# Performance work log

Measured on AMD Instinct MI355X. Metric: run time of the kernel, lower is better.

## Reference

```python
import jax, jax.numpy as jnp
import numpy as np

EMBED_DIM = 1024
ATTN_DIM = 1024
BATCH = 4
SEQ = 2048


def setup_inputs() -> dict:
    key = jax.random.key(0)
    k1, k2, k3, k4 = jax.random.split(key, 4)
    embedded = jax.random.normal(k1, (BATCH, SEQ, EMBED_DIM), dtype=jnp.float32)
    # torch Linear weights have shape [out_features, in_features]
    scale = 1.0 / np.sqrt(EMBED_DIM)
    W_K = jax.random.uniform(k2, (ATTN_DIM, EMBED_DIM), dtype=jnp.float32, minval=-scale, maxval=scale)
    W_Q = jax.random.uniform(k3, (ATTN_DIM, EMBED_DIM), dtype=jnp.float32, minval=-scale, maxval=scale)
    W_V = jax.random.uniform(k4, (ATTN_DIM, EMBED_DIM), dtype=jnp.float32, minval=-scale, maxval=scale)
    return {"embedded": embedded, "W_K": W_K, "W_Q": W_Q, "W_V": W_V}


def reference(embedded, W_K, W_Q, W_V):
    # embedded: [B, L, E]; W_*: [A, E] (torch Linear layout, applied as x @ W.T)
    L = embedded.shape[1]
    A = W_K.shape[0]
    K = jnp.einsum('ble,ae->bla', embedded, W_K)
    Q = jnp.einsum('ble,ae->bla', embedded, W_Q)
    V = jnp.einsum('ble,ae->bla', embedded, W_V)
    att = jnp.einsum('bqa,bka->bqk', Q, K) / jnp.sqrt(jnp.float32(A))  # [B, L, L]
    causal = jnp.tril(jnp.ones((L, L), dtype=bool))  # lower-triangular mask
    att = jnp.where(causal, att, -jnp.inf)
    att = jax.nn.softmax(att, axis=-1)
    return jnp.einsum('bqk,bka->bqa', att, V)
```

## Files before the change

kernel.cpp:

```cpp
#include <hip/hip_runtime.h>
#include <hip/hip_bf16.h>
#include <stdint.h>

#define BATCH 4
#define SEQ   2048
#define EMB   1024
#define ADIM  1024

typedef __attribute__((ext_vector_type(8))) short  short8;
typedef __attribute__((ext_vector_type(4))) float  float4v;

static __device__ __forceinline__ unsigned short f2bf(float f) {
    unsigned int u = __float_as_uint(f);
    u += 0x7FFFu + ((u >> 16) & 1u);
    return (unsigned short)(u >> 16);
}

static __device__ __forceinline__ uint2 pack4(float4v v) {
    uint2 r;
    r.x = (unsigned)f2bf(v.x) | ((unsigned)f2bf(v.y) << 16);
    r.y = (unsigned)f2bf(v.z) | ((unsigned)f2bf(v.w) << 16);
    return r;
}

static __device__ __forceinline__ void gload16(const void* g, void* l) {
    __builtin_amdgcn_global_load_lds(
        (const __attribute__((address_space(1))) void*)g,
        (__attribute__((address_space(3))) void*)l, 16, 0, 0);
}

static __device__ __forceinline__ int swz8(int row) { return ((row >> 1) & 3) << 3; }

__global__ __launch_bounds__(256) void prep_kernel(
    const float* __restrict__ X,  const float* __restrict__ Wv,
    const float* __restrict__ Wq, const float* __restrict__ Wk,
    unsigned short* __restrict__ Xb, unsigned short* __restrict__ Wvb,
    unsigned short* __restrict__ WqT, unsigned short* __restrict__ WkT,
    float* __restrict__ rowsum, float* __restrict__ out)
{
    __shared__ unsigned short T[64][72];
    const int bI = blockIdx.x;
    if (bI < 4608) {
        const float* src; unsigned short* dst; int off;
        if (bI < 4096) { src = X;  dst = Xb;  off = bI; }
        else           { src = Wv; dst = Wvb; off = bI - 4096; }
        const int i = (off * 256 + threadIdx.x) * 8;
        float4v a = *(const float4v*)(src + i);
        float4v b = *(const float4v*)(src + i + 4);
        uint2 pa = pack4(a), pb = pack4(b);
        uint4 o; o.x = pa.x; o.y = pa.y; o.z = pb.x; o.w = pb.y;
        *(uint4*)(dst + i) = o;
        return;
    }
    if (bI < 4616) {
        const int i = ((bI - 4608) * 256 + threadIdx.x) * 4;
        *(float4v*)(rowsum + i) = float4v{0.f, 0.f, 0.f, 0.f};
        return;
    }
    if (bI >= 5128) {
        const int o   = bI - 5128;
        const int b   = o >> 11;
        const int row = o & 2047;
        float* dst = out + ((size_t)(b * 2048 + row) * 1024) + threadIdx.x * 4;
        *(float4v*)dst = float4v{0.f, 0.f, 0.f, 0.f};
        return;
    }
    const int z    = (bI - 4616) >> 8;
    const int tile = (bI - 4616) & 255;
    const int ti = tile >> 4;
    const int tj = tile & 15;
    const float* W = z ? Wk : Wq;
    unsigned short* WT = z ? WkT : WqT;
    const int t  = threadIdx.x;
    const int r  = t >> 2;
    const int c  = (t & 3) << 4;

    const float* src = W + (size_t)(ti * 64 + r) * EMB + tj * 64 + c;
    #pragma unroll
    for (int u = 0; u < 4; ++u) {
        float4v v = *(const float4v*)(src + 4 * u);
        uint2 p = pack4(v);
        *(uint2*)&T[r][c + 4 * u] = p;
    }
    __syncthreads();
    unsigned short tmp[16];
    #pragma unroll
    for (int u = 0; u < 16; ++u) tmp[u] = T[c + u][r];
    unsigned short* dst = WT + (size_t)(tj * 64 + r) * EMB + ti * 64 + c;
    *(uint4*)(dst)     = *(uint4*)&tmp[0];
    *(uint4*)(dst + 8) = *(uint4*)&tmp[8];
}

static __device__ __forceinline__ void gemm_core(
    const unsigned short* __restrict__ A, const unsigned short* __restrict__ B,
    int lda, int ldb, int m0, int n0, int klen,
    unsigned short* As, unsigned short* Bs, float4v acc[4][4])
{
    const int tid  = threadIdx.x;
    const int r    = tid >> 2;
    const int c8   = ((tid & 3) << 3) ^ swz8(tid >> 2);
    const int lane = tid & 63;
    const int wave = tid >> 6;
    const int quad = lane >> 4;
    const int l16  = lane & 15;
    const int wm   = (wave >> 1) << 6;
    const int wn   = (wave & 1) << 6;

    const unsigned short* Ag = A + (size_t)(m0 + r) * lda + c8;
    const unsigned short* Bg = B + (size_t)(n0 + r) * ldb + c8;
    unsigned short* Al = As + tid * 8;
    unsigned short* Bl = Bs + tid * 8;
    const int niter = klen >> 5;

    #define ISSUE_A(k0, st) do { \
        unsigned short* al_ = Al + (st) * 4096; \
        gload16(Ag + (k0),                    al_); \
        gload16(Ag + (k0) + (size_t)64 * lda, al_ + 2048); \
    } while (0)
    #define ISSUE_B(k0, st) do { \
        unsigned short* bl_ = Bl + (st) * 4096; \
        gload16(Bg + (k0),                    bl_); \
        gload16(Bg + (k0) + (size_t)64 * ldb, bl_ + 2048); \
    } while (0)

    ISSUE_A(0, 0);  ISSUE_B(0, 0);
    ISSUE_A(32, 1); ISSUE_B(32, 1);

    int ci = 0, ii = 2;
    for (int it = 0; it < niter; ++it) {
        const int knext = (it + 2 < niter) ? ((it + 2) << 5) : 0;
        const unsigned short* Ah = As + ci * 4096;
        const unsigned short* Bh = Bs + ci * 4096;
        short8 bfr[4];

        ISSUE_A(knext, ii);
        asm volatile("s_waitcnt vmcnt(6)" ::: "memory");
        asm volatile("s_barrier" ::: "memory");
        {
            short8 af0, af1;
            {
                const int row = wm + l16;
                af0 = *(const short8*)&Ah[row * 32 + ((quad * 8) ^ swz8(row))];
            }
            {
                const int row = wm + 16 + l16;
                af1 = *(const short8*)&Ah[row * 32 + ((quad * 8) ^ swz8(row))];
            }
            #pragma unroll
            for (int j = 0; j < 4; ++j) {
                const int row = wn + 16 * j + l16;
                bfr[j] = *(const short8*)&Bh[row * 32 + ((quad * 8) ^ swz8(row))];
            }
            __builtin_amdgcn_s_setprio(1);
            #pragma unroll
            for (int j = 0; j < 4; ++j)
                acc[0][j] = __builtin_amdgcn_mfma_f32_16x16x32_bf16(af0, bfr[j], acc[0][j], 0, 0, 0);
            #pragma unroll
            for (int j = 0; j < 4; ++j)
                acc[1][j] = __builtin_amdgcn_mfma_f32_16x16x32_bf16(af1, bfr[j], acc[1][j], 0, 0, 0);
            __builtin_amdgcn_s_setprio(0);
        }
        asm volatile("s_barrier" ::: "memory");

        ISSUE_B(knext, ii);
        {
            short8 af2, af3;
            {
                const int row = wm + 32 + l16;
                af2 = *(const short8*)&Ah[row * 32 + ((quad * 8) ^ swz8(row))];
            }
            {
                const int row = wm + 48 + l16;
                af3 = *(const short8*)&Ah[row * 32 + ((quad * 8) ^ swz8(row))];
            }
            __builtin_amdgcn_s_setprio(1);
            #pragma unroll
            for (int j = 0; j < 4; ++j)
                acc[2][j] = __builtin_amdgcn_mfma_f32_16x16x32_bf16(af2, bfr[j], acc[2][j], 0, 0, 0);
            #pragma unroll
            for (int j = 0; j < 4; ++j)
                acc[3][j] = __builtin_amdgcn_mfma_f32_16x16x32_bf16(af3, bfr[j], acc[3][j], 0, 0, 0);
            __builtin_amdgcn_s_setprio(0);
        }
        asm volatile("s_barrier" ::: "memory");
        ci = (ci == 2) ? 0 : ci + 1;
        ii = (ii == 2) ? 0 : ii + 1;
    }
    asm volatile("s_waitcnt vmcnt(0)" ::: "memory");
    #undef ISSUE_A
    #undef ISSUE_B
}

#define DECL_TILE_IDX() \
    const int lane = threadIdx.x & 63; \
    const int wave = threadIdx.x >> 6; \
    const int quad = lane >> 4; \
    const int l16  = lane & 15; \
    const int wm   = (wave >> 1) << 6; \
    const int wn   = (wave & 1) << 6;

__global__ __launch_bounds__(256, 3) void m_kernel(
    const unsigned short* __restrict__ WkT, const unsigned short* __restrict__ WqT,
    float* __restrict__ Mtf)
{
    __shared__ __align__(16) unsigned short As[3 * 128 * 32];
    __shared__ __align__(16) unsigned short Bs[3 * 128 * 32];
    const int idx = blockIdx.x;
    const int kc  = idx >> 6;
    const int t   = idx & 63;
    const int m0  = (t >> 3) << 7;
    const int n0  = (t & 7) << 7;

    float4v acc[4][4];
    #pragma unroll
    for (int i = 0; i < 4; ++i)
        #pragma unroll
        for (int j = 0; j < 4; ++j)
            acc[i][j] = float4v{0.f, 0.f, 0.f, 0.f};

    gemm_core(WkT + kc * 256, WqT + kc * 256, EMB, EMB, m0, n0, 256, As, Bs, acc);

    float* dst = Mtf + (size_t)kc * 1024 * 1024;
    DECL_TILE_IDX();
    #pragma unroll
    for (int i = 0; i < 4; ++i)
        #pragma unroll
        for (int j = 0; j < 4; ++j)
            #pragma unroll
            for (int rr = 0; rr < 4; ++rr) {
                const int row = m0 + wm + 16 * i + quad * 4 + rr;
                const int col = n0 + wn + 16 * j + l16;
                dst[(size_t)row * EMB + col] = acc[i][j][rr];
            }
}

__global__ __launch_bounds__(256) void mc_kernel(
    const float* __restrict__ Mtf, unsigned short* __restrict__ Mt)
{
    const int base = (blockIdx.x * 256 + threadIdx.x) * 16;
    #pragma unroll
    for (int u = 0; u < 4; ++u) {
        const int i = base + u * 4;
        float4v s = *(const float4v*)(Mtf + i);
        s = s + *(const float4v*)(Mtf + 1048576 + i);
        s = s + *(const float4v*)(Mtf + 2097152 + i);
        s = s + *(const float4v*)(Mtf + 3145728 + i);
        s = s * 0.03125f;
        uint2 p = pack4(s);
        *(uint2*)(Mt + i) = p;
    }
}

__global__ __launch_bounds__(512, 2) void qv_kernel(
    const unsigned short* __restrict__ Xb, const unsigned short* __restrict__ Mt,
    const unsigned short* __restrict__ Wvb,
    unsigned short* __restrict__ Qpb, unsigned short* __restrict__ Vtb)
{
    __shared__ __align__(16) unsigned short LDS[49152];
    unsigned short* As = LDS;
    unsigned short* Bs = LDS + 24576;

    const int idx  = blockIdx.x;
    const int mt   = ((idx & 7) << 2) | ((idx >> 3) & 3);
    const int slot = idx >> 5;
    const int z    = slot >> 2;
    const int n0   = (slot & 3) << 8;
    const int m0   = mt << 8;
    const unsigned short* B = z ? Wvb : Mt;

    const int tid  = threadIdx.x;
    const int lane = tid & 63;
    const int wave = tid >> 6;
    const int quad = lane >> 4;
    const int l16  = lane & 15;
    const int wm   = (wave >> 2) << 7;
    const int wn   = (wave & 3) << 6;

    const int srow = tid >> 2;
    const int c8   = ((tid & 3) << 3) ^ swz8(srow);

    const unsigned short* Ag0 = Xb + (size_t)(m0 + srow) * EMB + c8;
    const unsigned short* Ag1 = Ag0 + (size_t)128 * EMB;
    const unsigned short* Bg0 = B  + (size_t)(n0 + srow) * EMB + c8;
    const unsigned short* Bg1 = Bg0 + (size_t)128 * EMB;
    unsigned short* Al = As + tid * 8;
    unsigned short* Bl = Bs + tid * 8;

    #define ISSUE_QA(t, st) do { \
        gload16(Ag0 + (t) * 32, Al + (st) * 8192); \
        gload16(Ag1 + (t) * 32, Al + (st) * 8192 + 4096); \
    } while (0)
    #define ISSUE_QB(t, st) do { \
        gload16(Bg0 + (t) * 32, Bl + (st) * 8192); \
        gload16(Bg1 + (t) * 32, Bl + (st) * 8192 + 4096); \
    } while (0)

    float4v acc[8][4];
    #pragma unroll
    for (int i = 0; i < 8; ++i)
        #pragma unroll
        for (int j = 0; j < 4; ++j)
            acc[i][j] = float4v{0.f, 0.f, 0.f, 0.f};

    ISSUE_QA(0, 0); ISSUE_QB(0, 0);
    ISSUE_QA(1, 1); ISSUE_QB(1, 1);

    int ci = 0, ii = 2;
    for (int it = 0; it < 32; ++it) {
        const int tn = (it + 2 < 32) ? (it + 2) : 0;
        const unsigned short* Ah = As + ci * 8192;
        const unsigned short* Bh = Bs + ci * 8192;
        short8 bfr[4];

        ISSUE_QA(tn, ii);
        asm volatile("s_waitcnt vmcnt(6)" ::: "memory");
        asm volatile("s_barrier" ::: "memory");
        {
            short8 af[4];
            #pragma unroll
            for (int i = 0; i < 4; ++i) {
                const int row = wm + 16 * i + l16;
                af[i] = *(const short8*)&Ah[row * 32 + ((quad * 8) ^ swz8(row))];
            }
            #pragma unroll
            for (int j = 0; j < 4; ++j) {
                const int row = wn + 16 * j + l16;
                bfr[j] = *(const short8*)&Bh[row * 32 + ((quad * 8) ^ swz8(row))];
            }
            __builtin_amdgcn_s_setprio(1);
            #pragma unroll
            for (int i = 0; i < 4; ++i)
                #pragma unroll
                for (int j = 0; j < 4; ++j)
                    acc[i][j] = __builtin_amdgcn_mfma_f32_16x16x32_bf16(af[i], bfr[j], acc[i][j], 0, 0, 0);
            __builtin_amdgcn_s_setprio(0);
        }
        asm volatile("s_barrier" ::: "memory");

        ISSUE_QB(tn, ii);
        {
            short8 af[4];
            #pragma unroll
            for (int i = 0; i < 4; ++i) {
                const int row = wm + 64 + 16 * i + l16;
                af[i] = *(const short8*)&Ah[row * 32 + ((quad * 8) ^ swz8(row))];
            }
            __builtin_amdgcn_s_setprio(1);
            #pragma unroll
            for (int i = 0; i < 4; ++i)
                #pragma unroll
                for (int j = 0; j < 4; ++j)
                    acc[i + 4][j] = __builtin_amdgcn_mfma_f32_16x16x32_bf16(af[i], bfr[j], acc[i + 4][j], 0, 0, 0);
            __builtin_amdgcn_s_setprio(0);
        }
        asm volatile("s_barrier" ::: "memory");
        ci = (ci == 2) ? 0 : ci + 1;
        ii = (ii == 2) ? 0 : ii + 1;
    }
    asm volatile("s_waitcnt vmcnt(0)" ::: "memory");
    #undef ISSUE_QA
    #undef ISSUE_QB

    if (z == 0) {
        #pragma unroll
        for (int i = 0; i < 8; ++i)
            #pragma unroll
            for (int j = 0; j < 4; ++j)
                #pragma unroll
                for (int rr = 0; rr < 4; ++rr) {
                    const int row = m0 + wm + ((i & 3) << 4) + ((i >> 2) << 6) + quad * 4 + rr;
                    const int col = n0 + wn + 16 * j + l16;
                    Qpb[(size_t)row * ADIM + col] = f2bf(acc[i][j][rr]);
                }
    } else {
        const int bb = m0 >> 11;
        const int l0 = m0 & (SEQ - 1);
        #pragma unroll
        for (int h = 0; h < 2; ++h) {
            __syncthreads();
            if ((wm >> 7) == h) {
                #pragma unroll
                for (int i = 0; i < 8; ++i)
                    #pragma unroll
                    for (int j = 0; j < 4; ++j) {
                        const int qloc = ((i & 3) << 4) + ((i >> 2) << 6) + quad * 4;
                        const int acol = wn + 16 * j + l16;
                        uint2 w;
                        w.x = (unsigned)f2bf(acc[i][j][0]) | ((unsigned)f2bf(acc[i][j][1]) << 16);
                        w.y = (unsigned)f2bf(acc[i][j][2]) | ((unsigned)f2bf(acc[i][j][3]) << 16);
                        *(uint2*)&LDS[acol * 136 + qloc] = w;
                    }
            }
            __syncthreads();
            const int acol = tid >> 1;
            const int qh   = (tid & 1) << 6;
            unsigned short* dst = Vtb + (((size_t)(bb * ADIM + n0 + acol)) << 11)
                                      + l0 + h * 128 + qh;
            #pragma unroll
            for (int u = 0; u < 8; ++u)
                *(uint4*)(dst + u * 8) = *(const uint4*)&LDS[acol * 136 + qh + u * 8];
        }
    }
}

__global__ __launch_bounds__(256, 3) void s_kernel(
    const unsigned short* __restrict__ Qpb, const unsigned short* __restrict__ Xb,
    unsigned short* __restrict__ E, float* __restrict__ rowsum)
{
    const int idx = blockIdx.x;
    const int x   = idx & 7;
    const int j   = idx >> 3;
    const int b   = j / 17;
    const int u   = j - b * 17;
    const int qt  = (u <= x) ? x : 15 - x;
    const int kt  = (u <= x) ? u : u - (x + 1);
    const int q0  = qt << 7;
    const int k0  = kt << 7;

    __shared__ __align__(16) unsigned short As[3 * 128 * 32];
    __shared__ __align__(16) unsigned short Bs[3 * 128 * 32];

    float4v acc[4][4];
    #pragma unroll
    for (int i = 0; i < 4; ++i)
        #pragma unroll
        for (int jj = 0; jj < 4; ++jj)
            acc[i][jj] = float4v{0.f, 0.f, 0.f, 0.f};

    gemm_core(Qpb + (size_t)b * SEQ * ADIM, Xb + (size_t)b * SEQ * EMB,
              ADIM, EMB, q0, k0, EMB, As, Bs, acc);

    unsigned short* Eb = E + (size_t)b * SEQ * SEQ;
    float* rsb = rowsum + (size_t)b * SEQ;
    DECL_TILE_IDX();
    #pragma unroll
    for (int i = 0; i < 4; ++i)
        #pragma unroll
        for (int rr = 0; rr < 4; ++rr) {
            const int row = q0 + wm + 16 * i + quad * 4 + rr;
            float s = 0.f;
            #pragma unroll
            for (int jj = 0; jj < 4; ++jj) {
                const int col = k0 + wn + 16 * jj + l16;
                float e = (col <= row) ? __expf(acc[i][jj][rr]) : 0.f;
                s += e;
                Eb[(size_t)row * SEQ + col] = f2bf(e);
            }
            s += __shfl_xor(s, 1);
            s += __shfl_xor(s, 2);
            s += __shfl_xor(s, 4);
            s += __shfl_xor(s, 8);
            if (l16 == 0) atomicAdd(&rsb[row], s);
        }
}

__global__ __launch_bounds__(256, 3) void pv_kernel(
    const unsigned short* __restrict__ E, const unsigned short* __restrict__ Vtb,
    const float* __restrict__ rowsum, float* __restrict__ out)
{
    const int idx = blockIdx.x;
    const int x   = idx & 7;
    const int j   = idx >> 3;
    const int c   = j >> 5;
    const int col = j & 31;
    const int b   = col >> 3;
    const int a0  = (col & 7) << 7;

    const int ea  = (x + 1) << 2;
    const int g0  = (c == 0) ? 0 : ((c == 1) ? 23 : 46);
    const int g1  = (c == 2) ? 68 : (g0 + 23);

    __shared__ __align__(16) unsigned short As[3 * 128 * 32];
    __shared__ __align__(16) unsigned short Bs[3 * 128 * 32];

    const unsigned short* Eb = E   + (size_t)b * SEQ * SEQ;
    const unsigned short* Vb = Vtb + (size_t)b * ADIM * SEQ;
    float* ob = out + (size_t)b * SEQ * ADIM;
    const float* rsb = rowsum + (size_t)b * SEQ;
    DECL_TILE_IDX();

    #pragma unroll
    for (int seg = 0; seg < 2; ++seg) {
        const int lo = seg ? ea : 0;
        const int hi = seg ? 68 : ea;
        const int s0 = (g0 > lo) ? g0 : lo;
        const int s1 = (g1 < hi) ? g1 : hi;
        if (s0 >= s1) continue;
        const int qt   = seg ? (15 - x) : x;
        const int q0   = qt << 7;
        const int kbeg = (s0 - lo) << 5;
        const int klen = (s1 - s0) << 5;

        float4v acc[4][4];
        #pragma unroll
        for (int i = 0; i < 4; ++i)
            #pragma unroll
            for (int jj = 0; jj < 4; ++jj)
                acc[i][jj] = float4v{0.f, 0.f, 0.f, 0.f};

        gemm_core(Eb + kbeg, Vb + kbeg, SEQ, SEQ, q0, a0, klen, As, Bs, acc);

        #pragma unroll
        for (int i = 0; i < 4; ++i)
            #pragma unroll
            for (int rr = 0; rr < 4; ++rr) {
                const int row = q0 + wm + 16 * i + quad * 4 + rr;
                const float inv = 1.0f / rsb[row];
                #pragma unroll
                for (int jj = 0; jj < 4; ++jj) {
                    const int col2 = a0 + wn + 16 * jj + l16;
                    atomicAdd(&ob[(size_t)row * ADIM + col2], acc[i][jj][rr] * inv);
                }
            }
        __syncthreads();
    }
}

extern "C" void kernel_launch(void* const* d_in, const int* in_sizes, int n_in,
                              void* d_out, int out_size, void* d_ws, size_t ws_size,
                              hipStream_t stream)
{
    const float* X  = (const float*)d_in[0];
    const float* Wk = (const float*)d_in[1];
    const float* Wq = (const float*)d_in[2];
    const float* Wv = (const float*)d_in[3];
    float* out = (float*)d_out;

    const size_t MB = 1024 * 1024;
    char* ws = (char*)d_ws;
    unsigned short* Xb  = (unsigned short*)(ws);
    unsigned short* Wvb = (unsigned short*)(ws + 16 * MB);
    unsigned short* WqT = (unsigned short*)(ws + 18 * MB);
    unsigned short* WkT = (unsigned short*)(ws + 20 * MB);
    unsigned short* Mt  = (unsigned short*)(ws + 22 * MB);
    unsigned short* Qpb = (unsigned short*)(ws + 24 * MB);
    unsigned short* E   = (unsigned short*)(ws + 40 * MB);
    unsigned short* Vtb = (unsigned short*)(ws + 72 * MB);
    float*          rowsum = (float*)(ws + 88 * MB);
    float*          Mtf = (float*)(ws + 40 * MB);

    hipLaunchKernelGGL(prep_kernel, dim3(13320), dim3(256), 0, stream,
                       X, Wv, Wq, Wk, Xb, Wvb, WqT, WkT, rowsum, out);
    hipLaunchKernelGGL(m_kernel, dim3(256), dim3(256), 0, stream, WkT, WqT, Mtf);
    hipLaunchKernelGGL(mc_kernel, dim3(256), dim3(256), 0, stream, Mtf, Mt);
    hipLaunchKernelGGL(qv_kernel, dim3(256), dim3(512), 0, stream,
                       Xb, Mt, Wvb, Qpb, Vtb);
    hipLaunchKernelGGL(s_kernel, dim3(544), dim3(256), 0, stream, Qpb, Xb, E, rowsum);
    hipLaunchKernelGGL(pv_kernel, dim3(768), dim3(256), 0, stream, E, Vtb, rowsum, out);
}
```

Measured before the change: 254.0 us.

## Rebalance causal PV split into two chunks and store upper rows directly

Changes the PV work split from three K-chunks to two. Blocks with c==0 handle the short first-half query tile outright, writing plain stores, plus part of the second-half tile. Blocks with c==1 take the remaining fixed 34-step chunk of the second-half tile. Because the first-half rows are now fully owned by one block, prep only zeroes the bottom half of the output, which reduces the prep grid and removes atomics for those rows. The trade-offs are uneven work per block and a grid cut from 768 to 512 blocks.

```diff
diff --git a/kernel.cpp b/kernel.cpp
--- a/kernel.cpp
+++ b/kernel.cpp
@@ -59,9 +59,10 @@
     }
     if (bI >= 5128) {
         const int o   = bI - 5128;
-        const int b   = o >> 11;
-        const int row = o & 2047;
-        float* dst = out + ((size_t)(b * 2048 + row) * 1024) + threadIdx.x * 4;
+        const int b   = o >> 10;
+        const int blk = o & 1023;
+        float* dst = out + ((size_t)(b * 2048 + 1024) * 1024)
+                         + (size_t)blk * 1024 + threadIdx.x * 4;
         *(float4v*)dst = float4v{0.f, 0.f, 0.f, 0.f};
         return;
     }
@@ -465,10 +466,7 @@
     const int col = j & 31;
     const int b   = col >> 3;
     const int a0  = (col & 7) << 7;
-
     const int ea  = (x + 1) << 2;
-    const int g0  = (c == 0) ? 0 : ((c == 1) ? 23 : 46);
-    const int g1  = (c == 2) ? 68 : (g0 + 23);
 
     __shared__ __align__(16) unsigned short As[3 * 128 * 32];
     __shared__ __align__(16) unsigned short Bs[3 * 128 * 32];
@@ -479,18 +477,59 @@
     const float* rsb = rowsum + (size_t)b * SEQ;
     DECL_TILE_IDX();
 
-    #pragma unroll
-    for (int seg = 0; seg < 2; ++seg) {
-        const int lo = seg ? ea : 0;
-        const int hi = seg ? 68 : ea;
-        const int s0 = (g0 > lo) ? g0 : lo;
-        const int s1 = (g1 < hi) ? g1 : hi;
-        if (s0 >= s1) continue;
-        const int qt   = seg ? (15 - x) : x;
-        const int q0   = qt << 7;
-        const int kbeg = (s0 - lo) << 5;
-        const int klen = (s1 - s0) << 5;
-
+    if (c == 0) {
+        {
+            const int q0 = x << 7;
+            float4v acc[4][4];
+            #pragma unroll
+            for (int i = 0; i < 4; ++i)
+                #pragma unroll
+                for (int jj = 0; jj < 4; ++jj)
+                    acc[i][jj] = float4v{0.f, 0.f, 0.f, 0.f};
+
+            gemm_core(Eb, Vb, SEQ, SEQ, q0, a0, ea << 5, As, Bs, acc);
+
+            #pragma unroll
+            for (int i = 0; i < 4; ++i)
+                #pragma unroll
+                for (int rr = 0; rr < 4; ++rr) {
+                    const int row = q0 + wm + 16 * i + quad * 4 + rr;
+                    const float inv = 1.0f / rsb[row];
+                    #pragma unroll
+                    for (int jj = 0; jj < 4; ++jj) {
+                        const int col2 = a0 + wn + 16 * jj + l16;
+                        ob[(size_t)row * ADIM + col2] = acc[i][jj][rr] * inv;
+                    }
+                }
+        }
+        __syncthreads();
+        {
+            const int q0 = (15 - x) << 7;
+            float4v acc[4][4];
+            #pragma unroll
+            for (int i = 0; i < 4; ++i)
+                #pragma unroll
+                for (int jj = 0; jj < 4; ++jj)
+                    acc[i][jj] = float4v{0.f, 0.f, 0.f, 0.f};
+
+            gemm_core(Eb, Vb, SEQ, SEQ, q0, a0, (34 - ea) << 5, As, Bs, acc);
+
+            #pragma unroll
+            for (int i = 0; i < 4; ++i)
+                #pragma unroll
+                for (int rr = 0; rr < 4; ++rr) {
+                    const int row = q0 + wm + 16 * i + quad * 4 + rr;
+                    const float inv = 1.0f / rsb[row];
+                    #pragma unroll
+                    for (int jj = 0; jj < 4; ++jj) {
+                        const int col2 = a0 + wn + 16 * jj + l16;
+                        atomicAdd(&ob[(size_t)row * ADIM + col2], acc[i][jj][rr] * inv);
+                    }
+                }
+        }
+    } else {
+        const int q0   = (15 - x) << 7;
+        const int kbeg = (34 - ea) << 5;
         float4v acc[4][4];
         #pragma unroll
         for (int i = 0; i < 4; ++i)
@@ -498,7 +537,7 @@
             for (int jj = 0; jj < 4; ++jj)
                 acc[i][jj] = float4v{0.f, 0.f, 0.f, 0.f};
 
-        gemm_core(Eb + kbeg, Vb + kbeg, SEQ, SEQ, q0, a0, klen, As, Bs, acc);
+        gemm_core(Eb + kbeg, Vb + kbeg, SEQ, SEQ, q0, a0, 34 << 5, As, Bs, acc);
 
         #pragma unroll
         for (int i = 0; i < 4; ++i)
@@ -512,7 +551,6 @@
                     atomicAdd(&ob[(size_t)row * ADIM + col2], acc[i][jj][rr] * inv);
                 }
             }
-        __syncthreads();
     }
 }
 
@@ -539,12 +577,12 @@
     float*          rowsum = (float*)(ws + 88 * MB);
     float*          Mtf = (float*)(ws + 40 * MB);
 
-    hipLaunchKernelGGL(prep_kernel, dim3(13320), dim3(256), 0, stream,
+    hipLaunchKernelGGL(prep_kernel, dim3(9224), dim3(256), 0, stream,
                        X, Wv, Wq, Wk, Xb, Wvb, WqT, WkT, rowsum, out);
     hipLaunchKernelGGL(m_kernel, dim3(256), dim3(256), 0, stream, WkT, WqT, Mtf);
     hipLaunchKernelGGL(mc_kernel, dim3(256), dim3(256), 0, stream, Mtf, Mt);
     hipLaunchKernelGGL(qv_kernel, dim3(256), dim3(512), 0, stream,
                        Xb, Mt, Wvb, Qpb, Vtb);
     hipLaunchKernelGGL(s_kernel, dim3(544), dim3(256), 0, stream, Qpb, Xb, E, rowsum);
-    hipLaunchKernelGGL(pv_kernel, dim3(768), dim3(256), 0, stream, E, Vtb, rowsum, out);
-}
+    hipLaunchKernelGGL(pv_kernel, dim3(512), dim3(256), 0, stream, E, Vtb, rowsum, out);
+}
```

New measurement: 240.5 us. -5.3%, faster.
